# Kernel tuning notes

Hardware: AMD Instinct MI355X
Metric: run time of the kernel (lower is better)

Reference implementation:

```python
import jax, jax.numpy as jnp
from jax import lax
import numpy as np

D_MODEL = 1024
N_HEADS = 16
D_STATE = D_MODEL // N_HEADS  # 64
EPS = 1e-6


def setup_inputs() -> dict:
    key = jax.random.key(0)
    ks = jax.random.split(key, 8)
    B, S = 4, 4096
    s = 1.0 / np.sqrt(D_MODEL)
    return {
        "x": jax.random.normal(ks[0], (B, S, D_MODEL), dtype=jnp.float32),
        "state": jnp.zeros((B, N_HEADS, D_STATE), dtype=jnp.float32),
        "norm_w": jnp.ones((D_MODEL,), dtype=jnp.float32),
        "Wp": jax.random.normal(ks[1], (D_MODEL, 3 * N_HEADS * D_STATE), dtype=jnp.float32) * s,
        "bp": jax.random.normal(ks[2], (3 * N_HEADS * D_STATE,), dtype=jnp.float32) * 0.01,
        "Wg": jax.random.normal(ks[3], (D_MODEL, D_MODEL), dtype=jnp.float32) * s,
        "bg": jax.random.normal(ks[4], (D_MODEL,), dtype=jnp.float32) * 0.01,
        "Wo": jax.random.normal(ks[5], (D_MODEL, D_MODEL), dtype=jnp.float32) * s,
        "bo": jax.random.normal(ks[6], (D_MODEL,), dtype=jnp.float32) * 0.01,
    }


def reference(x, state, norm_w, Wp, bp, Wg, bg, Wo, bo):
    B, S, D = x.shape
    # RMSNorm
    rms = jnp.sqrt(jnp.mean(x * x, axis=-1, keepdims=True) + EPS)
    xn = norm_w * x / rms
    # input-dependent gate and SSM parameters (all per-timestep, vectorized)
    gate = jax.nn.sigmoid(xn @ Wg + bg)                        # (B,S,D)
    p = (xn @ Wp + bp).reshape(B, S, N_HEADS, 3, D_STATE)
    delta = jax.nn.sigmoid(p[..., 0, :])                       # (B,S,H,Ds)
    Bt = p[..., 1, :]
    Ct = p[..., 2, :]
    # sequential recurrence h_{t+1} = delta_t * h_t + B_t via lax.scan over time
    def step(h, db):
        d, b = db
        h = d * h + b
        return h, h
    dT = jnp.moveaxis(delta, 1, 0)  # (S,B,H,Ds)
    bT = jnp.moveaxis(Bt, 1, 0)
    new_state, hs = lax.scan(step, state, (dT, bT))
    hs = jnp.moveaxis(hs, 0, 1)     # (B,S,H,Ds)
    ssm = (Ct * hs).reshape(B, S, D)
    mixed = gate * ssm + (1.0 - gate) * xn
    y = mixed @ Wo + bo + x         # out_proj + residual (dropout=0)
    return y, new_state
```

## Files before the change

### kernel.cpp

```cpp
#include <hip/hip_runtime.h>
#include <hip/hip_bf16.h>
#include <cstdint>
#include <cstddef>

#define D_MODEL 1024
#define N_HEADS 16
#define D_STATE 64
#define SEQ 4096
#define BATCH 4
#define M_TOK (BATCH * SEQ)
#define N1 4096
#define CLEN 128
#define NCH (SEQ / CLEN)
#define NCHAN (BATCH * D_MODEL)

typedef __attribute__((ext_vector_type(8))) short bf16x8;
typedef __attribute__((ext_vector_type(4))) float f32x4;

__device__ __forceinline__ float sigmoidf_(float x) {
    return 1.0f / (1.0f + __expf(-x));
}

__device__ __forceinline__ void async_load16(const void* g, void* l) {
    __builtin_amdgcn_global_load_lds(
        (__attribute__((address_space(1))) void*)(g),
        (__attribute__((address_space(3))) void*)(l), 16, 0, 0);
}

__global__ __launch_bounds__(256) void transpose_cvt(
    const float* __restrict__ src, __hip_bfloat16* __restrict__ dst,
    int K, int N)
{
    __shared__ float tile[32][33];
    int n0 = blockIdx.x * 32, k0 = blockIdx.y * 32;
    int tx = threadIdx.x, ty = threadIdx.y;
#pragma unroll
    for (int j = 0; j < 32; j += 8)
        tile[ty + j][tx] = src[(size_t)(k0 + ty + j) * N + n0 + tx];
    __syncthreads();
#pragma unroll
    for (int j = 0; j < 32; j += 8)
        dst[(size_t)(n0 + ty + j) * K + k0 + tx] = __float2bfloat16(tile[tx][ty + j]);
}

__global__ __launch_bounds__(256) void rmsnorm_kernel(
    const float* __restrict__ x, const float* __restrict__ w,
    __hip_bfloat16* __restrict__ xn)
{
    int m = blockIdx.x;
    int tid = threadIdx.x;
    const float4* xr = (const float4*)(x + (size_t)m * D_MODEL);
    float4 v = xr[tid];
    float ss = v.x * v.x + v.y * v.y + v.z * v.z + v.w * v.w;
#pragma unroll
    for (int o = 32; o >= 1; o >>= 1) ss += __shfl_xor(ss, o, 64);
    __shared__ float red[4];
    int wave = tid >> 6, lane = tid & 63;
    if (lane == 0) red[wave] = ss;
    __syncthreads();
    float tot = red[0] + red[1] + red[2] + red[3];
    float scale = rsqrtf(tot * (1.0f / D_MODEL) + 1e-6f);
    const float4* wr = (const float4*)w;
    float4 wv = wr[tid];
    __hip_bfloat16 o4[4];
    o4[0] = __float2bfloat16(wv.x * v.x * scale);
    o4[1] = __float2bfloat16(wv.y * v.y * scale);
    o4[2] = __float2bfloat16(wv.z * v.z * scale);
    o4[3] = __float2bfloat16(wv.w * v.w * scale);
    *(uint64_t*)(xn + (size_t)m * D_MODEL + tid * 4) = *(uint64_t*)o4;
}

template <int MODE>
__global__ __launch_bounds__(256) void gemm_bt(
    const __hip_bfloat16* __restrict__ A,
    const __hip_bfloat16* __restrict__ Bt,
    const float* __restrict__ bias0,
    const float* __restrict__ bias1,
    void* __restrict__ outp, int N, int K)
{
    __shared__ short As[128 * 32];
    __shared__ short Bs[128 * 32];
    const int tid = threadIdx.x;
    const int wave = tid >> 6, lane = tid & 63;
    const int m0 = blockIdx.y * 128, n0 = blockIdx.x * 128;
    const int wm = (wave >> 1) * 64, wn = (wave & 1) * 64;
    const int fr = lane & 15, fq = lane >> 4;

    f32x4 acc[4][4];
#pragma unroll
    for (int i = 0; i < 4; i++)
#pragma unroll
        for (int j = 0; j < 4; j++) acc[i][j] = (f32x4){0.f, 0.f, 0.f, 0.f};

    const int row = tid >> 2;
    const int kc = (tid & 3) * 8;
    const short* Ag = (const short*)A + (size_t)(m0 + row) * K + kc;
    const short* Bg = (const short*)Bt + (size_t)(n0 + row) * K + kc;
    short* AsW = As + tid * 8;
    short* BsW = Bs + tid * 8;

    for (int k0 = 0; k0 < K; k0 += 32) {
        async_load16(Ag, AsW);
        async_load16(Ag + (size_t)64 * K, AsW + 2048);
        async_load16(Bg, BsW);
        async_load16(Bg + (size_t)64 * K, BsW + 2048);
        Ag += 32; Bg += 32;
        __syncthreads();

        bf16x8 a[4], b[4];
#pragma unroll
        for (int i = 0; i < 4; i++)
            a[i] = *(const bf16x8*)&As[(wm + i * 16 + fr) * 32 + fq * 8];
#pragma unroll
        for (int j = 0; j < 4; j++)
            b[j] = *(const bf16x8*)&Bs[(wn + j * 16 + fr) * 32 + fq * 8];
#pragma unroll
        for (int i = 0; i < 4; i++)
#pragma unroll
            for (int j = 0; j < 4; j++)
                acc[i][j] = __builtin_amdgcn_mfma_f32_16x16x32_bf16(
                    a[i], b[j], acc[i][j], 0, 0, 0);
        __syncthreads();
    }

    if constexpr (MODE == 0) {
        __hip_bfloat16* O = (__hip_bfloat16*)outp;
#pragma unroll
        for (int i = 0; i < 4; i++)
#pragma unroll
            for (int r = 0; r < 4; r++) {
                int grow = m0 + wm + i * 16 + fq * 4 + r;
#pragma unroll
                for (int j = 0; j < 4; j++) {
                    int gcol = n0 + wn + j * 16 + fr;
                    float bv = (gcol < D_MODEL) ? bias0[gcol] : bias1[gcol - D_MODEL];
                    O[(size_t)grow * N + gcol] = __float2bfloat16(acc[i][j][r] + bv);
                }
            }
    } else {
        float* O = (float*)outp;
#pragma unroll
        for (int i = 0; i < 4; i++)
#pragma unroll
            for (int r = 0; r < 4; r++) {
                int grow = m0 + wm + i * 16 + fq * 4 + r;
#pragma unroll
                for (int j = 0; j < 4; j++) {
                    int gcol = n0 + wn + j * 16 + fr;
                    O[(size_t)grow * N + gcol] =
                        acc[i][j][r] + bias0[gcol] + bias1[(size_t)grow * D_MODEL + gcol];
                }
            }
    }
}

__global__ __launch_bounds__(256) void scan_part1(
    const __hip_bfloat16* __restrict__ out1,
    float* __restrict__ Abuf, float* __restrict__ Bbuf)
{
    int g = blockIdx.x * 256 + threadIdx.x;
    int chan = g & (NCHAN - 1);
    int c = g >> 12;
    int b = chan >> 10;
    int hd = chan & 1023;
    int h = hd >> 6, d = hd & 63;
    size_t tok0 = (size_t)b * SEQ + (size_t)c * CLEN;
    const __hip_bfloat16* pd = out1 + tok0 * N1 + D_MODEL + h * 192 + d;
    float a = 1.0f, hloc = 0.0f;
#pragma unroll 4
    for (int s = 0; s < CLEN; s++) {
        float dp = __bfloat162float(pd[0]);
        float bt = __bfloat162float(pd[64]);
        float sd = sigmoidf_(dp);
        a *= sd;
        hloc = sd * hloc + bt;
        pd += N1;
    }
    Abuf[c * NCHAN + chan] = a;
    Bbuf[c * NCHAN + chan] = hloc;
}

__global__ __launch_bounds__(256) void scan_comb(
    const float* __restrict__ Abuf, const float* __restrict__ Bbuf,
    const float* __restrict__ state, float* __restrict__ Pbuf,
    float* __restrict__ new_state)
{
    int chan = blockIdx.x * 256 + threadIdx.x;
    float hp = state[chan];
#pragma unroll
    for (int c = 0; c < NCH; c++) {
        Pbuf[c * NCHAN + chan] = hp;
        hp = Abuf[c * NCHAN + chan] * hp + Bbuf[c * NCHAN + chan];
    }
    new_state[chan] = hp;
}

__global__ __launch_bounds__(256) void scan_apply(
    const __hip_bfloat16* __restrict__ out1,
    const __hip_bfloat16* __restrict__ xn,
    const float* __restrict__ Pbuf,
    __hip_bfloat16* __restrict__ mixed)
{
    int g = blockIdx.x * 256 + threadIdx.x;
    int chan = g & (NCHAN - 1);
    int c = g >> 12;
    int b = chan >> 10;
    int hd = chan & 1023;
    int h = hd >> 6, d = hd & 63;
    size_t tok0 = (size_t)b * SEQ + (size_t)c * CLEN;
    const __hip_bfloat16* rbase = out1 + tok0 * N1;
    const __hip_bfloat16* xbase = xn + tok0 * D_MODEL + hd;
    __hip_bfloat16* mbase = mixed + tok0 * D_MODEL + hd;
    const int pcol = D_MODEL + h * 192 + d;
    float hh = Pbuf[c * NCHAN + chan];
#pragma unroll 4
    for (int s = 0; s < CLEN; s++) {
        const __hip_bfloat16* r = rbase + (size_t)s * N1;
        float dp = __bfloat162float(r[pcol]);
        float bt = __bfloat162float(r[pcol + 64]);
        float ct = __bfloat162float(r[pcol + 128]);
        float gp = __bfloat162float(r[hd]);
        float sd = sigmoidf_(dp);
        hh = sd * hh + bt;
        float gg = sigmoidf_(gp);
        float xv = __bfloat162float(xbase[(size_t)s * D_MODEL]);
        mbase[(size_t)s * D_MODEL] = __float2bfloat16(gg * (ct * hh) + (1.0f - gg) * xv);
    }
}

extern "C" void kernel_launch(void* const* d_in, const int* in_sizes, int n_in,
                              void* d_out, int out_size, void* d_ws, size_t ws_size,
                              hipStream_t stream) {
    const float* x      = (const float*)d_in[0];
    const float* state  = (const float*)d_in[1];
    const float* norm_w = (const float*)d_in[2];
    const float* Wp     = (const float*)d_in[3];
    const float* bp     = (const float*)d_in[4];
    const float* Wg     = (const float*)d_in[5];
    const float* bg     = (const float*)d_in[6];
    const float* Wo     = (const float*)d_in[7];
    const float* bo     = (const float*)d_in[8];
    float* out = (float*)d_out;

    __hip_bfloat16* W1T   = (__hip_bfloat16*)d_ws;
    __hip_bfloat16* WoT   = W1T + (size_t)N1 * D_MODEL;
    __hip_bfloat16* xnb   = WoT + (size_t)D_MODEL * D_MODEL;
    __hip_bfloat16* out1  = xnb + (size_t)M_TOK * D_MODEL;
    __hip_bfloat16* mixed = out1 + (size_t)M_TOK * N1;
    float* Abuf = (float*)(mixed + (size_t)M_TOK * D_MODEL);
    float* Bbuf = Abuf + (size_t)NCHAN * NCH;
    float* Pbuf = Bbuf + (size_t)NCHAN * NCH;

    dim3 tb(32, 8);
    transpose_cvt<<<dim3(1024 / 32, 1024 / 32), tb, 0, stream>>>(Wg, W1T, 1024, 1024);
    transpose_cvt<<<dim3(3072 / 32, 1024 / 32), tb, 0, stream>>>(
        Wp, W1T + (size_t)D_MODEL * D_MODEL, 1024, 3072);
    transpose_cvt<<<dim3(1024 / 32, 1024 / 32), tb, 0, stream>>>(Wo, WoT, 1024, 1024);

    rmsnorm_kernel<<<M_TOK, 256, 0, stream>>>(x, norm_w, xnb);

    gemm_bt<0><<<dim3(N1 / 128, M_TOK / 128), 256, 0, stream>>>(
        xnb, W1T, bg, bp, (void*)out1, N1, D_MODEL);

    scan_part1<<<(NCHAN * NCH) / 256, 256, 0, stream>>>(out1, Abuf, Bbuf);
    scan_comb<<<NCHAN / 256, 256, 0, stream>>>(
        Abuf, Bbuf, state, Pbuf, out + (size_t)M_TOK * D_MODEL);
    scan_apply<<<(NCHAN * NCH) / 256, 256, 0, stream>>>(out1, xnb, Pbuf, mixed);

    gemm_bt<1><<<dim3(D_MODEL / 128, M_TOK / 128), 256, 0, stream>>>(
        mixed, WoT, bo, x, (void*)out, D_MODEL, D_MODEL);
}
```

Measured before the change: 459.7 us.

## Replace 128x128 GEMM with 256x256 double-buffered swizzled-LDS MFMA kernel

Rewrites the bf16 GEMM to use 256x256 output tiles with 512 threads, K-step 64, and double-buffered async global-to-LDS loads with explicit vmcnt waits so the next tile's loads overlap compute. LDS rows are XOR-swizzled to avoid bank conflicts, workgroup IDs are remapped for L2 locality, and s_setprio brackets the MFMA bursts. This targets low data reuse and the exposed load latency of the old single-buffered 128x128 kernel. The cost is 128KB of dynamic LDS per block and heavy register use, which limit occupancy, plus fewer blocks for the smaller output GEMM.

```diff
diff --git a/kernel.cpp b/kernel.cpp
--- a/kernel.cpp
+++ b/kernel.cpp
@@ -70,87 +70,174 @@
     *(uint64_t*)(xn + (size_t)m * D_MODEL + tid * 4) = *(uint64_t*)o4;
 }
 
+
+__device__ __forceinline__ void stage8(const short*& Ag, const short*& Bg,
+                                       short* dbase, int stL, int K)
+{
+    short* la = dbase;
+    short* lb = dbase + 16384;
+#pragma unroll
+    for (int l = 0; l < 4; ++l) {
+        async_load16(Ag + (size_t)(l * 64) * K, la + stL + l * 4096);
+        async_load16(Bg + (size_t)(l * 64) * K, lb + stL + l * 4096);
+    }
+    Ag += 64;
+    Bg += 64;
+}
+
 template <int MODE>
-__global__ __launch_bounds__(256) void gemm_bt(
+__global__ __launch_bounds__(512, 2) void gemm256(
     const __hip_bfloat16* __restrict__ A,
     const __hip_bfloat16* __restrict__ Bt,
     const float* __restrict__ bias0,
     const float* __restrict__ bias1,
     void* __restrict__ outp, int N, int K)
 {
-    __shared__ short As[128 * 32];
-    __shared__ short Bs[128 * 32];
+    extern __shared__ short lds[];
     const int tid = threadIdx.x;
     const int wave = tid >> 6, lane = tid & 63;
-    const int m0 = blockIdx.y * 128, n0 = blockIdx.x * 128;
-    const int wm = (wave >> 1) * 64, wn = (wave & 1) * 64;
     const int fr = lane & 15, fq = lane >> 4;
-
-    f32x4 acc[4][4];
-#pragma unroll
-    for (int i = 0; i < 4; i++)
-#pragma unroll
-        for (int j = 0; j < 4; j++) acc[i][j] = (f32x4){0.f, 0.f, 0.f, 0.f};
-
-    const int row = tid >> 2;
-    const int kc = (tid & 3) * 8;
-    const short* Ag = (const short*)A + (size_t)(m0 + row) * K + kc;
-    const short* Bg = (const short*)Bt + (size_t)(n0 + row) * K + kc;
-    short* AsW = As + tid * 8;
-    short* BsW = Bs + tid * 8;
-
-    for (int k0 = 0; k0 < K; k0 += 32) {
-        async_load16(Ag, AsW);
-        async_load16(Ag + (size_t)64 * K, AsW + 2048);
-        async_load16(Bg, BsW);
-        async_load16(Bg + (size_t)64 * K, BsW + 2048);
-        Ag += 32; Bg += 32;
-        __syncthreads();
-
-        bf16x8 a[4], b[4];
-#pragma unroll
-        for (int i = 0; i < 4; i++)
-            a[i] = *(const bf16x8*)&As[(wm + i * 16 + fr) * 32 + fq * 8];
-#pragma unroll
-        for (int j = 0; j < 4; j++)
-            b[j] = *(const bf16x8*)&Bs[(wn + j * 16 + fr) * 32 + fq * 8];
-#pragma unroll
-        for (int i = 0; i < 4; i++)
-#pragma unroll
-            for (int j = 0; j < 4; j++)
-                acc[i][j] = __builtin_amdgcn_mfma_f32_16x16x32_bf16(
-                    a[i], b[j], acc[i][j], 0, 0, 0);
-        __syncthreads();
-    }
+    const int frx = fr & 7;
+    const int wm = (wave >> 2) * 128;
+    const int wn = (wave & 3) * 64;
+
+    const int gx = gridDim.x;
+    const int nwg = gx * gridDim.y;
+    const int orig = blockIdx.y * gx + blockIdx.x;
+    const int swz = (orig & 7) * (nwg >> 3) + (orig >> 3);
+    const int m0 = (swz / gx) * 256;
+    const int n0 = (swz % gx) * 256;
+
+    const int rb = tid >> 3, p8 = tid & 7;
+    const int lsl = p8 ^ (rb & 7);
+    const short* Ag = (const short*)A + (size_t)(m0 + rb) * K + lsl * 8;
+    const short* Bg = (const short*)Bt + (size_t)(n0 + rb) * K + lsl * 8;
+    const int stL = rb * 64 + p8 * 8;
+
+    const int NT = K >> 6;
+
+    f32x4 acc[2][4][4];
+#pragma unroll
+    for (int h = 0; h < 2; ++h)
+#pragma unroll
+        for (int i = 0; i < 4; ++i)
+#pragma unroll
+            for (int j = 0; j < 4; ++j)
+                acc[h][i][j] = (f32x4){0.f, 0.f, 0.f, 0.f};
+
+    stage8(Ag, Bg, lds, stL, K);
+    stage8(Ag, Bg, lds + 32768, stL, K);
+
+#define LDA(h, i, kk) (*(const bf16x8*)&Ab[(wm + (h)*64 + (i)*16 + fr) * 64 + \
+                                           (((kk)*4 + fq) ^ frx) * 8])
+#define LDB(j, kk)    (*(const bf16x8*)&Bb[(wn + (j)*16 + fr) * 64 + \
+                                           (((kk)*4 + fq) ^ frx) * 8])
+
+    for (int kt = 0; kt < NT; ++kt) {
+        if (kt + 1 < NT) { asm volatile("s_waitcnt vmcnt(8)" ::: "memory"); }
+        else             { asm volatile("s_waitcnt vmcnt(0)" ::: "memory"); }
+        __builtin_amdgcn_s_barrier();
+        __builtin_amdgcn_sched_barrier(0);
+
+        const short* Ab = lds + ((kt & 1) ? 32768 : 0);
+        const short* Bb = Ab + 16384;
+
+        bf16x8 af[4][2], b0[2][2], b1[2][2];
+
+#pragma unroll
+        for (int i = 0; i < 4; ++i) { af[i][0] = LDA(0, i, 0); af[i][1] = LDA(0, i, 1); }
+#pragma unroll
+        for (int j = 0; j < 2; ++j) { b0[j][0] = LDB(j, 0); b0[j][1] = LDB(j, 1); }
+        __builtin_amdgcn_s_setprio(1);
+#pragma unroll
+        for (int i = 0; i < 4; ++i)
+#pragma unroll
+            for (int j = 0; j < 2; ++j) {
+                acc[0][i][j] = __builtin_amdgcn_mfma_f32_16x16x32_bf16(af[i][0], b0[j][0], acc[0][i][j], 0, 0, 0);
+                acc[0][i][j] = __builtin_amdgcn_mfma_f32_16x16x32_bf16(af[i][1], b0[j][1], acc[0][i][j], 0, 0, 0);
+            }
+        __builtin_amdgcn_s_setprio(0);
+        __builtin_amdgcn_sched_barrier(0);
+
+#pragma unroll
+        for (int j = 0; j < 2; ++j) { b1[j][0] = LDB(2 + j, 0); b1[j][1] = LDB(2 + j, 1); }
+        __builtin_amdgcn_s_setprio(1);
+#pragma unroll
+        for (int i = 0; i < 4; ++i)
+#pragma unroll
+            for (int j = 0; j < 2; ++j) {
+                acc[0][i][2 + j] = __builtin_amdgcn_mfma_f32_16x16x32_bf16(af[i][0], b1[j][0], acc[0][i][2 + j], 0, 0, 0);
+                acc[0][i][2 + j] = __builtin_amdgcn_mfma_f32_16x16x32_bf16(af[i][1], b1[j][1], acc[0][i][2 + j], 0, 0, 0);
+            }
+        __builtin_amdgcn_s_setprio(0);
+        __builtin_amdgcn_sched_barrier(0);
+
+#pragma unroll
+        for (int i = 0; i < 4; ++i) { af[i][0] = LDA(1, i, 0); af[i][1] = LDA(1, i, 1); }
+        __builtin_amdgcn_s_setprio(1);
+#pragma unroll
+        for (int i = 0; i < 4; ++i)
+#pragma unroll
+            for (int j = 0; j < 2; ++j) {
+                acc[1][i][j] = __builtin_amdgcn_mfma_f32_16x16x32_bf16(af[i][0], b0[j][0], acc[1][i][j], 0, 0, 0);
+                acc[1][i][j] = __builtin_amdgcn_mfma_f32_16x16x32_bf16(af[i][1], b0[j][1], acc[1][i][j], 0, 0, 0);
+            }
+        __builtin_amdgcn_s_setprio(0);
+        __builtin_amdgcn_sched_barrier(0);
+
+        __builtin_amdgcn_s_setprio(1);
+#pragma unroll
+        for (int i = 0; i < 4; ++i)
+#pragma unroll
+            for (int j = 0; j < 2; ++j) {
+                acc[1][i][2 + j] = __builtin_amdgcn_mfma_f32_16x16x32_bf16(af[i][0], b1[j][0], acc[1][i][2 + j], 0, 0, 0);
+                acc[1][i][2 + j] = __builtin_amdgcn_mfma_f32_16x16x32_bf16(af[i][1], b1[j][1], acc[1][i][2 + j], 0, 0, 0);
+            }
+        __builtin_amdgcn_s_setprio(0);
+
+        __builtin_amdgcn_sched_barrier(0);
+        __builtin_amdgcn_s_barrier();
+        if (kt + 2 < NT) stage8(Ag, Bg, lds + ((kt & 1) ? 32768 : 0), stL, K);
+    }
+#undef LDA
+#undef LDB
 
     if constexpr (MODE == 0) {
         __hip_bfloat16* O = (__hip_bfloat16*)outp;
-#pragma unroll
-        for (int i = 0; i < 4; i++)
-#pragma unroll
-            for (int r = 0; r < 4; r++) {
-                int grow = m0 + wm + i * 16 + fq * 4 + r;
-#pragma unroll
-                for (int j = 0; j < 4; j++) {
-                    int gcol = n0 + wn + j * 16 + fr;
-                    float bv = (gcol < D_MODEL) ? bias0[gcol] : bias1[gcol - D_MODEL];
-                    O[(size_t)grow * N + gcol] = __float2bfloat16(acc[i][j][r] + bv);
+        float bv[4];
+#pragma unroll
+        for (int j = 0; j < 4; ++j) {
+            int gcol = n0 + wn + j * 16 + fr;
+            bv[j] = (gcol < D_MODEL) ? bias0[gcol] : bias1[gcol - D_MODEL];
+        }
+#pragma unroll
+        for (int h = 0; h < 2; ++h)
+#pragma unroll
+            for (int i = 0; i < 4; ++i)
+#pragma unroll
+                for (int r = 0; r < 4; ++r) {
+                    int grow = m0 + wm + h * 64 + i * 16 + fq * 4 + r;
+                    __hip_bfloat16* orow = O + (size_t)grow * N + n0 + wn + fr;
+#pragma unroll
+                    for (int j = 0; j < 4; ++j)
+                        orow[j * 16] = __float2bfloat16(acc[h][i][j][r] + bv[j]);
                 }
-            }
     } else {
         float* O = (float*)outp;
 #pragma unroll
-        for (int i = 0; i < 4; i++)
-#pragma unroll
-            for (int r = 0; r < 4; r++) {
-                int grow = m0 + wm + i * 16 + fq * 4 + r;
-#pragma unroll
-                for (int j = 0; j < 4; j++) {
-                    int gcol = n0 + wn + j * 16 + fr;
-                    O[(size_t)grow * N + gcol] =
-                        acc[i][j][r] + bias0[gcol] + bias1[(size_t)grow * D_MODEL + gcol];
+        for (int h = 0; h < 2; ++h)
+#pragma unroll
+            for (int i = 0; i < 4; ++i)
+#pragma unroll
+                for (int r = 0; r < 4; ++r) {
+                    int grow = m0 + wm + h * 64 + i * 16 + fq * 4 + r;
+#pragma unroll
+                    for (int j = 0; j < 4; ++j) {
+                        int gcol = n0 + wn + j * 16 + fr;
+                        O[(size_t)grow * N + gcol] =
+                            acc[h][i][j][r] + bias0[gcol] + bias1[(size_t)grow * D_MODEL + gcol];
+                    }
                 }
-            }
     }
 }
 
@@ -251,6 +338,15 @@
     float* Bbuf = Abuf + (size_t)NCHAN * NCH;
     float* Pbuf = Bbuf + (size_t)NCHAN * NCH;
 
+    static bool attr_set = false;
+    if (!attr_set) {
+        hipFuncSetAttribute(reinterpret_cast<const void*>(&gemm256<0>),
+                            hipFuncAttributeMaxDynamicSharedMemorySize, 131072);
+        hipFuncSetAttribute(reinterpret_cast<const void*>(&gemm256<1>),
+                            hipFuncAttributeMaxDynamicSharedMemorySize, 131072);
+        attr_set = true;
+    }
+
     dim3 tb(32, 8);
     transpose_cvt<<<dim3(1024 / 32, 1024 / 32), tb, 0, stream>>>(Wg, W1T, 1024, 1024);
     transpose_cvt<<<dim3(3072 / 32, 1024 / 32), tb, 0, stream>>>(
@@ -259,7 +355,7 @@
 
     rmsnorm_kernel<<<M_TOK, 256, 0, stream>>>(x, norm_w, xnb);
 
-    gemm_bt<0><<<dim3(N1 / 128, M_TOK / 128), 256, 0, stream>>>(
+    gemm256<0><<<dim3(N1 / 256, M_TOK / 256), 512, 131072, stream>>>(
         xnb, W1T, bg, bp, (void*)out1, N1, D_MODEL);
 
     scan_part1<<<(NCHAN * NCH) / 256, 256, 0, stream>>>(out1, Abuf, Bbuf);
@@ -267,6 +363,6 @@
         Abuf, Bbuf, state, Pbuf, out + (size_t)M_TOK * D_MODEL);
     scan_apply<<<(NCHAN * NCH) / 256, 256, 0, stream>>>(out1, xnb, Pbuf, mixed);
 
-    gemm_bt<1><<<dim3(D_MODEL / 128, M_TOK / 128), 256, 0, stream>>>(
+    gemm256<1><<<dim3(D_MODEL / 256, M_TOK / 256), 512, 131072, stream>>>(
         mixed, WoT, bo, x, (void*)out, D_MODEL, D_MODEL);
 }
```

New measurement: 391.4 us. 14.8% less time.
